# Performance work log

Hardware: AMD Instinct MI355X
Metric: run time of the kernel (lower is better)

Reference implementation:

```python
import jax, jax.numpy as jnp
import numpy as np

B, M, E, K = 8, 256, 128, 16
H, A, R, RMS = 1024, 256, 1024, 512
NEG = -1e25


def setup_inputs() -> dict:
    key = jax.random.key(0)
    ks = jax.random.split(key, 12)
    inp = {
        "mention_reprs": jax.random.normal(ks[0], (B, M, H), jnp.float32),
        "entities": jax.random.randint(ks[1], (B, E, K), 0, M),
        "entity_masks": jax.random.randint(ks[2], (B, E, K), 0, 2, dtype=jnp.int32),
        "relation_memory": jax.random.normal(ks[3], (R, RMS), jnp.float32),
        # GatedMILAttention params
        "Wv": jax.random.normal(ks[4], (A, H), jnp.float32) / np.sqrt(H),
        "bv": jnp.zeros((A,), jnp.float32),
        "Wu": jax.random.normal(ks[5], (A, H), jnp.float32) / np.sqrt(H),
        "bu": jnp.zeros((A,), jnp.float32),
        "Wa": jax.random.normal(ks[6], (1, A), jnp.float32) / np.sqrt(A),
        "ba": jnp.zeros((1,), jnp.float32),
        # relation memory read linear: Linear(RMS, H)
        "Wr": jax.random.normal(ks[7], (H, RMS), jnp.float32) / np.sqrt(RMS),
        "br": jnp.zeros((H,), jnp.float32),
        # output linear: Linear(H + RMS, H)
        "Wo": jax.random.normal(ks[8], (H, H + RMS), jnp.float32) / np.sqrt(H + RMS),
        "bo": jnp.zeros((H,), jnp.float32),
    }
    return inp


def reference(mention_reprs, entities, entity_masks, relation_memory,
              Wv, bv, Wu, bu, Wa, ba, Wr, br, Wo, bo):
    # gather mention clusters: [B, E, K, H]
    clusters = jax.vmap(lambda m, e: m[e])(mention_reprs, entities)
    # gated MIL attention
    aV = jnp.tanh(jnp.einsum('bekh,ah->beka', clusters, Wv) + bv)
    aU = jax.nn.sigmoid(jnp.einsum('bekh,ah->beka', clusters, Wu) + bu)
    logits = jnp.einsum('beka,oa->beko', aV * aU, Wa) + ba  # [B,E,K,1]
    mask = entity_masks[..., None].astype(bool)
    logits = jnp.where(mask, logits, NEG)
    a = jax.nn.softmax(logits, axis=2)
    # weighted pooling over mentions: [B, E, H]
    entity_reprs = jnp.sum(a * clusters, axis=2)
    # relation memory read (memory detached for the read projection)
    s_w = jax.lax.stop_gradient(relation_memory) @ Wr.T + br        # [R, H]
    s = jnp.einsum('beh,rh->ber', entity_reprs, s_w)                # [B, E, R]
    s = jnp.einsum('ber,rm->bem', s, relation_memory)               # [B, E, RMS]
    out = jnp.concatenate([entity_reprs, s], axis=-1) @ Wo.T + bo   # [B, E, H]
    return out  # dropout is identity at inference
```

## Files before the change

### kernel.cpp

```cpp
#include <hip/hip_runtime.h>
#include <cstdint>
#include <cstddef>

#define NEG_ (-1e25f)

typedef __bf16 bf16x8 __attribute__((ext_vector_type(8)));
typedef float  f32x4  __attribute__((ext_vector_type(4)));
typedef short  s16x8  __attribute__((ext_vector_type(8)));
typedef const __attribute__((address_space(1))) void* gas_t;
typedef __attribute__((address_space(3))) void* las_t;

#define MFMA16 __builtin_amdgcn_mfma_f32_16x16x32_bf16

__device__ __forceinline__ short f2bf(float f) {
  union { float f; unsigned u; } v; v.f = f;
  unsigned r = v.u + 0x7fffu + ((v.u >> 16) & 1u);
  return (short)(r >> 16);
}

__device__ __forceinline__ s16x8 cvt8(const float* s) {
  bf16x8 r;
  #pragma unroll
  for (int j = 0; j < 8; ++j) r[j] = (__bf16)s[j];
  union { bf16x8 b; s16x8 s; } u; u.b = r; return u.s;
}

struct Params {
  const float* ment; const int* ents; const int* msk;
  const float* rm; const float* Wv; const float* bv; const float* Wu;
  const float* bu; const float* Wa; const float* Wr; const float* br;
  const float* Wo; const float* bo; float* out;
  short *Xb, *Wvb, *Wub, *rmb, *Wrb, *Wo2b, *swTb, *Ub, *Weffb, *erb;
  float *wpart, *cf, *gw2;
};

__global__ __launch_bounds__(256) void k0(Params p) {
  const int g = blockIdx.x * 256 + threadIdx.x;
  #pragma unroll
  for (int it = 0; it < 4; ++it) {
    int u = g + it * 131072;
    long e = (long)u * 8;
    const float* src; short* dst;
    if (u < 262144)      { src = p.ment + e;                     dst = p.Xb + e; }
    else if (u < 294912) { long o = e - 2097152; src = p.Wv + o; dst = p.Wvb + o; }
    else if (u < 327680) { long o = e - 2359296; src = p.Wu + o; dst = p.Wub + o; }
    else if (u < 393216) { long o = e - 2621440; src = p.rm + o; dst = p.rmb + o; }
    else if (u < 458752) { long o = e - 3145728; src = p.Wr + o; dst = p.Wrb + o; }
    else                 { long o = e - 3670016;
                           src = p.Wo + (o >> 9) * 1536 + 1024 + (o & 511);
                           dst = p.Wo2b + o; }
    float t[8];
    *(float4*)t       = *(const float4*)src;
    *(float4*)(t + 4) = *(const float4*)(src + 4);
    *(s16x8*)dst = cvt8(t);
  }
}

__device__ void bgemm_dual(const short* __restrict__ A1, const short* __restrict__ A2,
                           long lda, const short* __restrict__ B, long ldb,
                           short* __restrict__ C1, short* __restrict__ C2, int ldc,
                           int NT, int m0, int n0, short* lds) {
  short* As1 = lds;
  short* As2 = lds + 4 * 2048;
  short* Bs  = lds + 8 * 2048;
  const int tid = threadIdx.x, wave = tid >> 6, lane = tid & 63;
  const int quad = lane >> 4, l16 = lane & 15;
  const int wm = (wave & 1) * 32, wn = (wave >> 1) * 32;
  const int srow = tid >> 2, scol = (tid & 3) * 8;
  const short* A1g = A1 + (long)(m0 + srow) * lda + scol;
  const short* A2g = A2 + (long)(m0 + srow) * lda + scol;
  const short* Bg  = B  + (long)(n0 + srow) * ldb + scol;
  const int ldsoff = wave * 512;
  auto issue = [&](int kt) {
    int buf = kt & 3; int ko = kt * 32;
    __builtin_amdgcn_global_load_lds((gas_t)(A1g + ko), (las_t)(As1 + buf * 2048 + ldsoff), 16, 0, 0);
    __builtin_amdgcn_global_load_lds((gas_t)(A2g + ko), (las_t)(As2 + buf * 2048 + ldsoff), 16, 0, 0);
    __builtin_amdgcn_global_load_lds((gas_t)(Bg  + ko), (las_t)(Bs  + buf * 2048 + ldsoff), 16, 0, 0);
  };
  f32x4 acc1[2][2] = {}, acc2[2][2] = {};
  issue(0); issue(1); issue(2);
  for (int kt = 0; kt < NT; ++kt) {
    int rem = NT - 1 - kt;
    if (rem >= 2)      asm volatile("s_waitcnt vmcnt(6)" ::: "memory");
    else if (rem == 1) asm volatile("s_waitcnt vmcnt(3)" ::: "memory");
    else               asm volatile("s_waitcnt vmcnt(0)" ::: "memory");
    asm volatile("s_barrier" ::: "memory");
    if (kt + 3 < NT) issue(kt + 3);
    const short* as1 = As1 + (kt & 3) * 2048;
    const short* as2 = As2 + (kt & 3) * 2048;
    const short* bs  = Bs  + (kt & 3) * 2048;
    bf16x8 a10 = *(const bf16x8*)&as1[(wm + l16) * 32 + quad * 8];
    bf16x8 a11 = *(const bf16x8*)&as1[(wm + 16 + l16) * 32 + quad * 8];
    bf16x8 a20 = *(const bf16x8*)&as2[(wm + l16) * 32 + quad * 8];
    bf16x8 a21 = *(const bf16x8*)&as2[(wm + 16 + l16) * 32 + quad * 8];
    bf16x8 b0  = *(const bf16x8*)&bs[(wn + l16) * 32 + quad * 8];
    bf16x8 b1  = *(const bf16x8*)&bs[(wn + 16 + l16) * 32 + quad * 8];
    acc1[0][0] = MFMA16(a10, b0, acc1[0][0], 0, 0, 0);
    acc1[0][1] = MFMA16(a10, b1, acc1[0][1], 0, 0, 0);
    acc1[1][0] = MFMA16(a11, b0, acc1[1][0], 0, 0, 0);
    acc1[1][1] = MFMA16(a11, b1, acc1[1][1], 0, 0, 0);
    acc2[0][0] = MFMA16(a20, b0, acc2[0][0], 0, 0, 0);
    acc2[0][1] = MFMA16(a20, b1, acc2[0][1], 0, 0, 0);
    acc2[1][0] = MFMA16(a21, b0, acc2[1][0], 0, 0, 0);
    acc2[1][1] = MFMA16(a21, b1, acc2[1][1], 0, 0, 0);
  }
  #pragma unroll
  for (int i = 0; i < 2; ++i)
    #pragma unroll
    for (int j = 0; j < 2; ++j) {
      int col = n0 + wn + j * 16 + l16;
      #pragma unroll
      for (int r = 0; r < 4; ++r) {
        int row = m0 + wm + i * 16 + quad * 4 + r;
        C1[(long)row * ldc + col] = f2bf(acc1[i][j][r]);
        C2[(long)row * ldc + col] = f2bf(acc2[i][j][r]);
      }
    }
}

template <int EPI>
__device__ void bgemm64(const short* __restrict__ A, int lda,
                        const short* __restrict__ B, int ldb,
                        void* __restrict__ C, int ldc, int NT, int m0, int n0,
                        const float* __restrict__ e0, const float* __restrict__ e1,
                        const float* __restrict__ e2, short* lds) {
  short* As = lds;
  short* Bs = lds + 4 * 2048;
  const int tid = threadIdx.x;
  const int wave = tid >> 6, lane = tid & 63;
  const int quad = lane >> 4, l16 = lane & 15;
  const int wm = (wave & 1) * 32, wn = (wave >> 1) * 32;
  const int srow = tid >> 2, scol = (tid & 3) * 8;
  const short* Ag = A + (long)(m0 + srow) * lda + scol;
  const short* Bg = B + (long)(n0 + srow) * ldb + scol;
  const int ldsoff = wave * 512;
  auto issue = [&](int kt) {
    int buf = kt & 3; int ko = kt * 32;
    __builtin_amdgcn_global_load_lds((gas_t)(Ag + ko), (las_t)(As + buf * 2048 + ldsoff), 16, 0, 0);
    __builtin_amdgcn_global_load_lds((gas_t)(Bg + ko), (las_t)(Bs + buf * 2048 + ldsoff), 16, 0, 0);
  };
  f32x4 acc[2][2] = {};
  issue(0); issue(1); issue(2);
  for (int kt = 0; kt < NT; ++kt) {
    int rem = NT - 1 - kt;
    if (rem >= 2)      asm volatile("s_waitcnt vmcnt(4)" ::: "memory");
    else if (rem == 1) asm volatile("s_waitcnt vmcnt(2)" ::: "memory");
    else               asm volatile("s_waitcnt vmcnt(0)" ::: "memory");
    asm volatile("s_barrier" ::: "memory");
    if (kt + 3 < NT) issue(kt + 3);
    const short* as = As + (kt & 3) * 2048;
    const short* bs = Bs + (kt & 3) * 2048;
    bf16x8 a0 = *(const bf16x8*)&as[(wm + l16) * 32 + quad * 8];
    bf16x8 a1 = *(const bf16x8*)&as[(wm + 16 + l16) * 32 + quad * 8];
    bf16x8 b0 = *(const bf16x8*)&bs[(wn + l16) * 32 + quad * 8];
    bf16x8 b1 = *(const bf16x8*)&bs[(wn + 16 + l16) * 32 + quad * 8];
    acc[0][0] = MFMA16(a0, b0, acc[0][0], 0, 0, 0);
    acc[0][1] = MFMA16(a0, b1, acc[0][1], 0, 0, 0);
    acc[1][0] = MFMA16(a1, b0, acc[1][0], 0, 0, 0);
    acc[1][1] = MFMA16(a1, b1, acc[1][1], 0, 0, 0);
  }
  #pragma unroll
  for (int i = 0; i < 2; ++i)
    #pragma unroll
    for (int j = 0; j < 2; ++j) {
      int col = n0 + wn + j * 16 + l16;
      #pragma unroll
      for (int r = 0; r < 4; ++r) {
        int row = m0 + wm + i * 16 + quad * 4 + r;
        float v = acc[i][j][r];
        if constexpr (EPI == 1) {
          v += e0[(long)row * 1536 + col];
          ((short*)C)[(long)row * ldc + col] = f2bf(v);
        } else {
          v += e0[col] + e1[row] * e2[col];
          ((float*)C)[(long)row * ldc + col] = v;
        }
      }
    }
}

__device__ void vu_ring(int mi, int ni, const Params& p, short* lds, float* red) {
  short* As  = lds;
  short* Bvs = lds + 4 * 1024;
  short* Bus = lds + 4 * 1024 + 4 * 2048;
  const int tid = threadIdx.x, wave = tid >> 6, lane = tid & 63;
  const int quad = lane >> 4, l16 = lane & 15;
  const int wm = (wave & 1) * 16, wn = (wave >> 1) * 32;
  const int m0 = mi * 32, n0 = ni * 64;
  const int srow = tid >> 2, scol = (tid & 3) * 8;
  const short* Ag  = p.Xb  + (long)(m0 + srow) * 1024 + scol;
  const short* Bvg = p.Wvb + (long)(n0 + srow) * 1024 + scol;
  const short* Bug = p.Wub + (long)(n0 + srow) * 1024 + scol;
  const int ldsoff = wave * 512;
  auto issue = [&](int kt) {
    int buf = kt & 3; int ko = kt * 32;
    if (wave < 2)
      __builtin_amdgcn_global_load_lds((gas_t)(Ag + ko), (las_t)(As + buf * 1024 + ldsoff), 16, 0, 0);
    __builtin_amdgcn_global_load_lds((gas_t)(Bvg + ko), (las_t)(Bvs + buf * 2048 + ldsoff), 16, 0, 0);
    __builtin_amdgcn_global_load_lds((gas_t)(Bug + ko), (las_t)(Bus + buf * 2048 + ldsoff), 16, 0, 0);
  };
  f32x4 accv[2] = {}, accu[2] = {};
  issue(0); issue(1); issue(2);
  for (int kt = 0; kt < 32; ++kt) {
    int rem = 31 - kt;
    if (wave < 2) {
      if (rem >= 2)      asm volatile("s_waitcnt vmcnt(6)" ::: "memory");
      else if (rem == 1) asm volatile("s_waitcnt vmcnt(3)" ::: "memory");
      else               asm volatile("s_waitcnt vmcnt(0)" ::: "memory");
    } else {
      if (rem >= 2)      asm volatile("s_waitcnt vmcnt(4)" ::: "memory");
      else if (rem == 1) asm volatile("s_waitcnt vmcnt(2)" ::: "memory");
      else               asm volatile("s_waitcnt vmcnt(0)" ::: "memory");
    }
    asm volatile("s_barrier" ::: "memory");
    if (kt + 3 < 32) issue(kt + 3);
    const short* as  = As  + (kt & 3) * 1024;
    const short* bvs = Bvs + (kt & 3) * 2048;
    const short* bus = Bus + (kt & 3) * 2048;
    bf16x8 af = *(const bf16x8*)&as[(wm + l16) * 32 + quad * 8];
    bf16x8 v0 = *(const bf16x8*)&bvs[(wn + l16) * 32 + quad * 8];
    bf16x8 v1 = *(const bf16x8*)&bvs[(wn + 16 + l16) * 32 + quad * 8];
    bf16x8 u0 = *(const bf16x8*)&bus[(wn + l16) * 32 + quad * 8];
    bf16x8 u1 = *(const bf16x8*)&bus[(wn + 16 + l16) * 32 + quad * 8];
    accv[0] = MFMA16(af, v0, accv[0], 0, 0, 0);
    accv[1] = MFMA16(af, v1, accv[1], 0, 0, 0);
    accu[0] = MFMA16(af, u0, accu[0], 0, 0, 0);
    accu[1] = MFMA16(af, u1, accu[1], 0, 0, 0);
  }
  float wsum[4] = {0.f, 0.f, 0.f, 0.f};
  #pragma unroll
  for (int j = 0; j < 2; ++j) {
    int col = n0 + wn + j * 16 + l16;
    float bvc = p.bv[col], buc = p.bu[col], wac = p.Wa[col];
    #pragma unroll
    for (int r = 0; r < 4; ++r) {
      float vv = tanhf(accv[j][r] + bvc);
      float uu = accu[j][r] + buc;
      wsum[r] += (vv / (1.0f + expf(-uu))) * wac;
    }
  }
  #pragma unroll
  for (int r = 0; r < 4; ++r) {
    float s = wsum[r];
    s += __shfl_down(s, 8, 16);
    s += __shfl_down(s, 4, 16);
    s += __shfl_down(s, 2, 16);
    s += __shfl_down(s, 1, 16);
    if (l16 == 0) red[(wave >> 1) * 32 + wm + quad * 4 + r] = s;
  }
  __syncthreads();
  if (tid < 32) p.wpart[ni * 2048 + m0 + tid] = red[tid] + red[32 + tid];
}

__device__ void gw2_wave(int row, const Params& p) {
  const int lane = threadIdx.x & 63;
  const short* u = p.Ub + (long)row * 1024 + lane * 16;
  union { s16x8 s; bf16x8 b; } w0, w1;
  w0.s = *(const s16x8*)u;
  w1.s = *(const s16x8*)(u + 8);
  float s = 0.f;
  #pragma unroll
  for (int j = 0; j < 8; ++j) s += (float)w0.b[j] + (float)w1.b[j];
  #pragma unroll
  for (int off = 32; off > 0; off >>= 1) s += __shfl_down(s, off);
  if (lane == 0) p.gw2[row] = s;
}

__device__ void entity_wave(int be, const Params& p) {
  const int lane = threadIdx.x & 63;
  const int b = be >> 7;
  float a = NEG_; int idx = 0;
  if (lane < 16) {
    idx = p.ents[be * 16 + lane];
    int j = (b << 8) + idx;
    float lw = p.wpart[j] + p.wpart[2048 + j] + p.wpart[4096 + j] + p.wpart[6144 + j];
    a = p.msk[be * 16 + lane] ? lw : NEG_;
  }
  float m = a;
  m = fmaxf(m, __shfl_xor(m, 1, 16));
  m = fmaxf(m, __shfl_xor(m, 2, 16));
  m = fmaxf(m, __shfl_xor(m, 4, 16));
  m = fmaxf(m, __shfl_xor(m, 8, 16));
  float e = expf(a - m);
  float s = e;
  s += __shfl_xor(s, 1, 16);
  s += __shfl_xor(s, 2, 16);
  s += __shfl_xor(s, 4, 16);
  s += __shfl_xor(s, 8, 16);
  float aw = e / s;
  const float* Xr = p.ment + ((long)b << 18);
  const int h0 = lane * 16;
  float acc[16];
  #pragma unroll
  for (int t = 0; t < 16; ++t) acc[t] = 0.f;
  #pragma unroll
  for (int k = 0; k < 16; ++k) {
    float ak = __shfl(aw, k);
    int   ik = __shfl(idx, k);
    const float* xr = Xr + (long)ik * 1024 + h0;
    f32x4 x0 = *(const f32x4*)(xr);
    f32x4 x1 = *(const f32x4*)(xr + 4);
    f32x4 x2 = *(const f32x4*)(xr + 8);
    f32x4 x3 = *(const f32x4*)(xr + 12);
    #pragma unroll
    for (int t = 0; t < 4; ++t) {
      acc[t]      += ak * x0[t];
      acc[4 + t]  += ak * x1[t];
      acc[8 + t]  += ak * x2[t];
      acc[12 + t] += ak * x3[t];
    }
  }
  short* er = p.erb + (long)be * 1024 + h0;
  *(s16x8*)er       = cvt8(acc);
  *(s16x8*)(er + 8) = cvt8(acc + 8);
  float c = 0.f;
  const float* brp = p.br + h0;
  #pragma unroll
  for (int t = 0; t < 16; ++t) c += acc[t] * brp[t];
  #pragma unroll
  for (int off = 32; off > 0; off >>= 1) c += __shfl_down(c, off);
  if (lane == 0) p.cf[be] = c;
}

__global__ __launch_bounds__(256) void k1(Params p) {
  __shared__ short lds[24576];
  __shared__ float red[64];
  const int blk = blockIdx.x;
  if (blk < 256) {
    bgemm_dual(p.Wrb, p.Wo2b, 512, p.rmb, 512, p.swTb, p.Ub, 1024, 16,
               (blk >> 4) * 64, (blk & 15) * 64, lds);
  } else {
    int q = blk - 256;
    vu_ring(q & 63, q >> 6, p, lds, red);
  }
}

__global__ __launch_bounds__(256) void k2(Params p) {
  __shared__ short lds[16384];
  const int blk = blockIdx.x;
  if (blk < 256) {
    bgemm64<1>(p.Ub, 1024, p.swTb, 1024, p.Weffb, 1024, 32,
               (blk >> 4) * 64, (blk & 15) * 64, p.Wo, nullptr, nullptr, lds);
  } else {
    int q = blk - 256;
    int wave = threadIdx.x >> 6;
    gw2_wave(q * 4 + wave, p);
    entity_wave(q * 4 + wave, p);
  }
}

__global__ __launch_bounds__(256) void k3(Params p) {
  __shared__ short lds[16384];
  const int blk = blockIdx.x;
  bgemm64<2>(p.erb, 1024, p.Weffb, 1024, p.out, 1024, 32,
             (blk >> 4) * 64, (blk & 15) * 64, p.bo, p.cf, p.gw2, lds);
}

extern "C" void kernel_launch(void* const* d_in, const int* in_sizes, int n_in,
                              void* d_out, int out_size, void* d_ws, size_t ws_size,
                              hipStream_t stream) {
  (void)in_sizes; (void)n_in; (void)out_size; (void)ws_size;
  Params p;
  p.ment = (const float*)d_in[0];
  p.ents = (const int*)d_in[1];
  p.msk  = (const int*)d_in[2];
  p.rm   = (const float*)d_in[3];
  p.Wv   = (const float*)d_in[4];
  p.bv   = (const float*)d_in[5];
  p.Wu   = (const float*)d_in[6];
  p.bu   = (const float*)d_in[7];
  p.Wa   = (const float*)d_in[8];
  p.Wr   = (const float*)d_in[10];
  p.br   = (const float*)d_in[11];
  p.Wo   = (const float*)d_in[12];
  p.bo   = (const float*)d_in[13];
  p.out  = (float*)d_out;

  char* w = (char*)d_ws;
  auto alloc = [&](size_t bytes) {
    void* q = (void*)w; w += (bytes + 255) & ~(size_t)255; return q;
  };
  p.Xb    = (short*)alloc((size_t)2048 * 1024 * 2);
  p.Wvb   = (short*)alloc((size_t)256 * 1024 * 2);
  p.Wub   = (short*)alloc((size_t)256 * 1024 * 2);
  p.rmb   = (short*)alloc((size_t)1024 * 512 * 2);
  p.Wrb   = (short*)alloc((size_t)1024 * 512 * 2);
  p.Wo2b  = (short*)alloc((size_t)1024 * 512 * 2);
  p.swTb  = (short*)alloc((size_t)1024 * 1024 * 2);
  p.Ub    = (short*)alloc((size_t)1024 * 1024 * 2);
  p.Weffb = (short*)alloc((size_t)1024 * 1024 * 2);
  p.erb   = (short*)alloc((size_t)1024 * 1024 * 2);
  p.wpart = (float*)alloc((size_t)4 * 2048 * 4);
  p.cf    = (float*)alloc((size_t)1024 * 4);
  p.gw2   = (float*)alloc((size_t)1024 * 4);

  k0<<<512, 256, 0, stream>>>(p);
  k1<<<512, 256, 0, stream>>>(p);
  k2<<<512, 256, 0, stream>>>(p);
  k3<<<256, 256, 0, stream>>>(p);
}
```

Before: 138.2 us.

## Fuse three dependent kernels into one persistent kernel with grid barriers

Merges k1, k2 and k3 into a single kernel, kF, that separates the stages with a software grid-wide barrier built from an atomic counter and a generation word. k0 resets the barrier state before kF runs. The aim is to remove two kernel launch gaps and the tail drain between stages. In exchange it needs all 512 blocks resident at once, which launch_bounds(256,2) and the larger LDS allocation must allow, otherwise it deadlocks. Half the blocks sit idle during the last GEMM stage.

```diff
diff --git a/kernel.cpp b/kernel.cpp
--- a/kernel.cpp
+++ b/kernel.cpp
@@ -32,9 +32,31 @@
   const float* Wo; const float* bo; float* out;
   short *Xb, *Wvb, *Wub, *rmb, *Wrb, *Wo2b, *swTb, *Ub, *Weffb, *erb;
   float *wpart, *cf, *gw2;
+  unsigned* bar;
 };
 
+__device__ __forceinline__ void gridbar(unsigned* bar, unsigned nb) {
+  __syncthreads();
+  if (threadIdx.x == 0) {
+    unsigned* cnt = bar;
+    unsigned* gen = bar + 16;
+    unsigned g = __hip_atomic_load(gen, __ATOMIC_RELAXED, __HIP_MEMORY_SCOPE_AGENT);
+    __threadfence();
+    unsigned v = __hip_atomic_fetch_add(cnt, 1u, __ATOMIC_ACQ_REL, __HIP_MEMORY_SCOPE_AGENT);
+    if (v == nb - 1u) {
+      __hip_atomic_store(cnt, 0u, __ATOMIC_RELAXED, __HIP_MEMORY_SCOPE_AGENT);
+      __hip_atomic_store(gen, g + 1u, __ATOMIC_RELEASE, __HIP_MEMORY_SCOPE_AGENT);
+    } else {
+      while (__hip_atomic_load(gen, __ATOMIC_ACQUIRE, __HIP_MEMORY_SCOPE_AGENT) == g)
+        __builtin_amdgcn_s_sleep(2);
+    }
+    __threadfence();
+  }
+  __syncthreads();
+}
+
 __global__ __launch_bounds__(256) void k0(Params p) {
+  if (blockIdx.x == 0 && threadIdx.x == 0) { p.bar[0] = 0u; p.bar[16] = 0u; }
   const int g = blockIdx.x * 256 + threadIdx.x;
   #pragma unroll
   for (int it = 0; it < 4; ++it) {
@@ -322,10 +344,11 @@
   if (lane == 0) p.cf[be] = c;
 }
 
-__global__ __launch_bounds__(256) void k1(Params p) {
+__global__ __launch_bounds__(256, 2) void kF(Params p) {
   __shared__ short lds[24576];
   __shared__ float red[64];
   const int blk = blockIdx.x;
+
   if (blk < 256) {
     bgemm_dual(p.Wrb, p.Wo2b, 512, p.rmb, 512, p.swTb, p.Ub, 1024, 16,
                (blk >> 4) * 64, (blk & 15) * 64, lds);
@@ -333,11 +356,8 @@
     int q = blk - 256;
     vu_ring(q & 63, q >> 6, p, lds, red);
   }
-}
-
-__global__ __launch_bounds__(256) void k2(Params p) {
-  __shared__ short lds[16384];
-  const int blk = blockIdx.x;
+  gridbar(p.bar, 512);
+
   if (blk < 256) {
     bgemm64<1>(p.Ub, 1024, p.swTb, 1024, p.Weffb, 1024, 32,
                (blk >> 4) * 64, (blk & 15) * 64, p.Wo, nullptr, nullptr, lds);
@@ -347,13 +367,12 @@
     gw2_wave(q * 4 + wave, p);
     entity_wave(q * 4 + wave, p);
   }
-}
-
-__global__ __launch_bounds__(256) void k3(Params p) {
-  __shared__ short lds[16384];
-  const int blk = blockIdx.x;
-  bgemm64<2>(p.erb, 1024, p.Weffb, 1024, p.out, 1024, 32,
-             (blk >> 4) * 64, (blk & 15) * 64, p.bo, p.cf, p.gw2, lds);
+  gridbar(p.bar, 512);
+
+  if (blk < 256) {
+    bgemm64<2>(p.erb, 1024, p.Weffb, 1024, p.out, 1024, 32,
+               (blk >> 4) * 64, (blk & 15) * 64, p.bo, p.cf, p.gw2, lds);
+  }
 }
 
 extern "C" void kernel_launch(void* const* d_in, const int* in_sizes, int n_in,
@@ -393,9 +412,8 @@
   p.wpart = (float*)alloc((size_t)4 * 2048 * 4);
   p.cf    = (float*)alloc((size_t)1024 * 4);
   p.gw2   = (float*)alloc((size_t)1024 * 4);
+  p.bar   = (unsigned*)alloc(256);
 
   k0<<<512, 256, 0, stream>>>(p);
-  k1<<<512, 256, 0, stream>>>(p);
-  k2<<<512, 256, 0, stream>>>(p);
-  k3<<<256, 256, 0, stream>>>(p);
-}
+  kF<<<512, 256, 0, stream>>>(p);
+}
```

New measurement: 366.4 us. 2.65x slower.

## Switch GEMMs to 128x128 tiles with 3-stage pipeline and enlarge VU tile

Applied to the files above, without the earlier changes.

Replaces the 64x64 GEMM tiles (and the dual-output GEMM) with a single 128x128 tile kernel where each wave computes a 64x64 sub-tile with a 3-buffer async LDS pipeline, and splits the dual GEMM into separate blocks. The gated attention GEMM tile grows from 32 rows to 128 rows. This raises MFMA work per LDS load and cuts global traffic, but reduces block counts (e.g. k3 to 64 blocks on a 256-CU GPU), risking underutilization and higher register pressure.

```diff
diff --git a/kernel.cpp b/kernel.cpp
--- a/kernel.cpp
+++ b/kernel.cpp
@@ -23,6 +23,10 @@
   #pragma unroll
   for (int j = 0; j < 8; ++j) r[j] = (__bf16)s[j];
   union { bf16x8 b; s16x8 s; } u; u.b = r; return u.s;
+}
+
+__device__ __forceinline__ void gload(const short* g, short* l) {
+  __builtin_amdgcn_global_load_lds((gas_t)g, (las_t)l, 16, 0, 0);
 }
 
 struct Params {
@@ -56,119 +60,63 @@
   }
 }
 
-__device__ void bgemm_dual(const short* __restrict__ A1, const short* __restrict__ A2,
-                           long lda, const short* __restrict__ B, long ldb,
-                           short* __restrict__ C1, short* __restrict__ C2, int ldc,
-                           int NT, int m0, int n0, short* lds) {
-  short* As1 = lds;
-  short* As2 = lds + 4 * 2048;
-  short* Bs  = lds + 8 * 2048;
+template <int NT, int EPI>
+__device__ void mm128(const short* __restrict__ A, int lda,
+                      const short* __restrict__ B, int ldb,
+                      void* __restrict__ C, int ldc, int m0, int n0,
+                      const float* __restrict__ e0, const float* __restrict__ e1,
+                      const float* __restrict__ e2, short* lds) {
+  short* As = lds;
+  short* Bs = lds + 12288;
   const int tid = threadIdx.x, wave = tid >> 6, lane = tid & 63;
   const int quad = lane >> 4, l16 = lane & 15;
-  const int wm = (wave & 1) * 32, wn = (wave >> 1) * 32;
-  const int srow = tid >> 2, scol = (tid & 3) * 8;
-  const short* A1g = A1 + (long)(m0 + srow) * lda + scol;
-  const short* A2g = A2 + (long)(m0 + srow) * lda + scol;
-  const short* Bg  = B  + (long)(n0 + srow) * ldb + scol;
-  const int ldsoff = wave * 512;
-  auto issue = [&](int kt) {
-    int buf = kt & 3; int ko = kt * 32;
-    __builtin_amdgcn_global_load_lds((gas_t)(A1g + ko), (las_t)(As1 + buf * 2048 + ldsoff), 16, 0, 0);
-    __builtin_amdgcn_global_load_lds((gas_t)(A2g + ko), (las_t)(As2 + buf * 2048 + ldsoff), 16, 0, 0);
-    __builtin_amdgcn_global_load_lds((gas_t)(Bg  + ko), (las_t)(Bs  + buf * 2048 + ldsoff), 16, 0, 0);
-  };
-  f32x4 acc1[2][2] = {}, acc2[2][2] = {};
-  issue(0); issue(1); issue(2);
-  for (int kt = 0; kt < NT; ++kt) {
-    int rem = NT - 1 - kt;
-    if (rem >= 2)      asm volatile("s_waitcnt vmcnt(6)" ::: "memory");
-    else if (rem == 1) asm volatile("s_waitcnt vmcnt(3)" ::: "memory");
-    else               asm volatile("s_waitcnt vmcnt(0)" ::: "memory");
-    asm volatile("s_barrier" ::: "memory");
-    if (kt + 3 < NT) issue(kt + 3);
-    const short* as1 = As1 + (kt & 3) * 2048;
-    const short* as2 = As2 + (kt & 3) * 2048;
-    const short* bs  = Bs  + (kt & 3) * 2048;
-    bf16x8 a10 = *(const bf16x8*)&as1[(wm + l16) * 32 + quad * 8];
-    bf16x8 a11 = *(const bf16x8*)&as1[(wm + 16 + l16) * 32 + quad * 8];
-    bf16x8 a20 = *(const bf16x8*)&as2[(wm + l16) * 32 + quad * 8];
-    bf16x8 a21 = *(const bf16x8*)&as2[(wm + 16 + l16) * 32 + quad * 8];
-    bf16x8 b0  = *(const bf16x8*)&bs[(wn + l16) * 32 + quad * 8];
-    bf16x8 b1  = *(const bf16x8*)&bs[(wn + 16 + l16) * 32 + quad * 8];
-    acc1[0][0] = MFMA16(a10, b0, acc1[0][0], 0, 0, 0);
-    acc1[0][1] = MFMA16(a10, b1, acc1[0][1], 0, 0, 0);
-    acc1[1][0] = MFMA16(a11, b0, acc1[1][0], 0, 0, 0);
-    acc1[1][1] = MFMA16(a11, b1, acc1[1][1], 0, 0, 0);
-    acc2[0][0] = MFMA16(a20, b0, acc2[0][0], 0, 0, 0);
-    acc2[0][1] = MFMA16(a20, b1, acc2[0][1], 0, 0, 0);
-    acc2[1][0] = MFMA16(a21, b0, acc2[1][0], 0, 0, 0);
-    acc2[1][1] = MFMA16(a21, b1, acc2[1][1], 0, 0, 0);
-  }
-  #pragma unroll
-  for (int i = 0; i < 2; ++i)
-    #pragma unroll
-    for (int j = 0; j < 2; ++j) {
-      int col = n0 + wn + j * 16 + l16;
-      #pragma unroll
-      for (int r = 0; r < 4; ++r) {
-        int row = m0 + wm + i * 16 + quad * 4 + r;
-        C1[(long)row * ldc + col] = f2bf(acc1[i][j][r]);
-        C2[(long)row * ldc + col] = f2bf(acc2[i][j][r]);
-      }
-    }
-}
-
-template <int EPI>
-__device__ void bgemm64(const short* __restrict__ A, int lda,
-                        const short* __restrict__ B, int ldb,
-                        void* __restrict__ C, int ldc, int NT, int m0, int n0,
-                        const float* __restrict__ e0, const float* __restrict__ e1,
-                        const float* __restrict__ e2, short* lds) {
-  short* As = lds;
-  short* Bs = lds + 4 * 2048;
-  const int tid = threadIdx.x;
-  const int wave = tid >> 6, lane = tid & 63;
-  const int quad = lane >> 4, l16 = lane & 15;
-  const int wm = (wave & 1) * 32, wn = (wave >> 1) * 32;
+  const int wm = (wave & 1) * 64, wn = (wave >> 1) * 64;
   const int srow = tid >> 2, scol = (tid & 3) * 8;
   const short* Ag = A + (long)(m0 + srow) * lda + scol;
   const short* Bg = B + (long)(n0 + srow) * ldb + scol;
-  const int ldsoff = wave * 512;
+  const int wb = wave * 512;
   auto issue = [&](int kt) {
-    int buf = kt & 3; int ko = kt * 32;
-    __builtin_amdgcn_global_load_lds((gas_t)(Ag + ko), (las_t)(As + buf * 2048 + ldsoff), 16, 0, 0);
-    __builtin_amdgcn_global_load_lds((gas_t)(Bg + ko), (las_t)(Bs + buf * 2048 + ldsoff), 16, 0, 0);
+    int buf = kt % 3; int ko = kt * 32;
+    gload(Ag + ko,            As + buf * 4096 + wb);
+    gload(Ag + 64 * lda + ko, As + buf * 4096 + 2048 + wb);
+    gload(Bg + ko,            Bs + buf * 4096 + wb);
+    gload(Bg + 64 * ldb + ko, Bs + buf * 4096 + 2048 + wb);
   };
-  f32x4 acc[2][2] = {};
-  issue(0); issue(1); issue(2);
+  f32x4 acc[4][4] = {};
+  issue(0); issue(1);
+  #pragma unroll
   for (int kt = 0; kt < NT; ++kt) {
-    int rem = NT - 1 - kt;
-    if (rem >= 2)      asm volatile("s_waitcnt vmcnt(4)" ::: "memory");
-    else if (rem == 1) asm volatile("s_waitcnt vmcnt(2)" ::: "memory");
-    else               asm volatile("s_waitcnt vmcnt(0)" ::: "memory");
+    if (kt < NT - 1) asm volatile("s_waitcnt vmcnt(4)" ::: "memory");
+    else             asm volatile("s_waitcnt vmcnt(0)" ::: "memory");
     asm volatile("s_barrier" ::: "memory");
-    if (kt + 3 < NT) issue(kt + 3);
-    const short* as = As + (kt & 3) * 2048;
-    const short* bs = Bs + (kt & 3) * 2048;
-    bf16x8 a0 = *(const bf16x8*)&as[(wm + l16) * 32 + quad * 8];
-    bf16x8 a1 = *(const bf16x8*)&as[(wm + 16 + l16) * 32 + quad * 8];
-    bf16x8 b0 = *(const bf16x8*)&bs[(wn + l16) * 32 + quad * 8];
-    bf16x8 b1 = *(const bf16x8*)&bs[(wn + 16 + l16) * 32 + quad * 8];
-    acc[0][0] = MFMA16(a0, b0, acc[0][0], 0, 0, 0);
-    acc[0][1] = MFMA16(a0, b1, acc[0][1], 0, 0, 0);
-    acc[1][0] = MFMA16(a1, b0, acc[1][0], 0, 0, 0);
-    acc[1][1] = MFMA16(a1, b1, acc[1][1], 0, 0, 0);
-  }
-  #pragma unroll
-  for (int i = 0; i < 2; ++i)
-    #pragma unroll
-    for (int j = 0; j < 2; ++j) {
+    if (kt + 2 < NT) issue(kt + 2);
+    const short* as = As + (kt % 3) * 4096;
+    const short* bs = Bs + (kt % 3) * 4096;
+    bf16x8 a[4], b[4];
+    #pragma unroll
+    for (int i = 0; i < 4; ++i)
+      a[i] = *(const bf16x8*)&as[(wm + i * 16 + l16) * 32 + quad * 8];
+    #pragma unroll
+    for (int j = 0; j < 4; ++j)
+      b[j] = *(const bf16x8*)&bs[(wn + j * 16 + l16) * 32 + quad * 8];
+    #pragma unroll
+    for (int i = 0; i < 4; ++i)
+      #pragma unroll
+      for (int j = 0; j < 4; ++j)
+        acc[i][j] = MFMA16(a[i], b[j], acc[i][j], 0, 0, 0);
+  }
+  #pragma unroll
+  for (int i = 0; i < 4; ++i)
+    #pragma unroll
+    for (int j = 0; j < 4; ++j) {
       int col = n0 + wn + j * 16 + l16;
       #pragma unroll
       for (int r = 0; r < 4; ++r) {
         int row = m0 + wm + i * 16 + quad * 4 + r;
         float v = acc[i][j][r];
-        if constexpr (EPI == 1) {
+        if constexpr (EPI == 0) {
+          ((short*)C)[(long)row * ldc + col] = f2bf(v);
+        } else if constexpr (EPI == 1) {
           v += e0[(long)row * 1536 + col];
           ((short*)C)[(long)row * ldc + col] = f2bf(v);
         } else {
@@ -179,77 +127,86 @@
     }
 }
 
-__device__ void vu_ring(int mi, int ni, const Params& p, short* lds, float* red) {
+__device__ void mmvu(int q, const Params& p, short* lds, float* red) {
   short* As  = lds;
-  short* Bvs = lds + 4 * 1024;
-  short* Bus = lds + 4 * 1024 + 4 * 2048;
+  short* Bvs = lds + 12288;
+  short* Bus = lds + 12288 + 6144;
+  const int mi = q >> 2, ni = q & 3;
+  const int m0 = mi * 128, n0 = ni * 64;
   const int tid = threadIdx.x, wave = tid >> 6, lane = tid & 63;
   const int quad = lane >> 4, l16 = lane & 15;
-  const int wm = (wave & 1) * 16, wn = (wave >> 1) * 32;
-  const int m0 = mi * 32, n0 = ni * 64;
+  const int wm = (wave & 1) * 64, wn = (wave >> 1) * 32;
   const int srow = tid >> 2, scol = (tid & 3) * 8;
   const short* Ag  = p.Xb  + (long)(m0 + srow) * 1024 + scol;
   const short* Bvg = p.Wvb + (long)(n0 + srow) * 1024 + scol;
   const short* Bug = p.Wub + (long)(n0 + srow) * 1024 + scol;
-  const int ldsoff = wave * 512;
+  const int wb = wave * 512;
   auto issue = [&](int kt) {
-    int buf = kt & 3; int ko = kt * 32;
-    if (wave < 2)
-      __builtin_amdgcn_global_load_lds((gas_t)(Ag + ko), (las_t)(As + buf * 1024 + ldsoff), 16, 0, 0);
-    __builtin_amdgcn_global_load_lds((gas_t)(Bvg + ko), (las_t)(Bvs + buf * 2048 + ldsoff), 16, 0, 0);
-    __builtin_amdgcn_global_load_lds((gas_t)(Bug + ko), (las_t)(Bus + buf * 2048 + ldsoff), 16, 0, 0);
+    int buf = kt % 3; int ko = kt * 32;
+    gload(Ag + ko,             As + buf * 4096 + wb);
+    gload(Ag + 64 * 1024 + ko, As + buf * 4096 + 2048 + wb);
+    gload(Bvg + ko,            Bvs + buf * 2048 + wb);
+    gload(Bug + ko,            Bus + buf * 2048 + wb);
   };
-  f32x4 accv[2] = {}, accu[2] = {};
-  issue(0); issue(1); issue(2);
+  f32x4 av[4][2] = {}, au[4][2] = {};
+  issue(0); issue(1);
+  #pragma unroll
   for (int kt = 0; kt < 32; ++kt) {
-    int rem = 31 - kt;
-    if (wave < 2) {
-      if (rem >= 2)      asm volatile("s_waitcnt vmcnt(6)" ::: "memory");
-      else if (rem == 1) asm volatile("s_waitcnt vmcnt(3)" ::: "memory");
-      else               asm volatile("s_waitcnt vmcnt(0)" ::: "memory");
-    } else {
-      if (rem >= 2)      asm volatile("s_waitcnt vmcnt(4)" ::: "memory");
-      else if (rem == 1) asm volatile("s_waitcnt vmcnt(2)" ::: "memory");
-      else               asm volatile("s_waitcnt vmcnt(0)" ::: "memory");
+    if (kt < 31) asm volatile("s_waitcnt vmcnt(4)" ::: "memory");
+    else         asm volatile("s_waitcnt vmcnt(0)" ::: "memory");
+    asm volatile("s_barrier" ::: "memory");
+    if (kt + 2 < 32) issue(kt + 2);
+    const short* as  = As  + (kt % 3) * 4096;
+    const short* bvs = Bvs + (kt % 3) * 2048;
+    const short* bus = Bus + (kt % 3) * 2048;
+    bf16x8 a[4], bv_[2], bu_[2];
+    #pragma unroll
+    for (int i = 0; i < 4; ++i)
+      a[i] = *(const bf16x8*)&as[(wm + i * 16 + l16) * 32 + quad * 8];
+    #pragma unroll
+    for (int j = 0; j < 2; ++j) {
+      bv_[j] = *(const bf16x8*)&bvs[(wn + j * 16 + l16) * 32 + quad * 8];
+      bu_[j] = *(const bf16x8*)&bus[(wn + j * 16 + l16) * 32 + quad * 8];
     }
-    asm volatile("s_barrier" ::: "memory");
-    if (kt + 3 < 32) issue(kt + 3);
-    const short* as  = As  + (kt & 3) * 1024;
-    const short* bvs = Bvs + (kt & 3) * 2048;
-    const short* bus = Bus + (kt & 3) * 2048;
-    bf16x8 af = *(const bf16x8*)&as[(wm + l16) * 32 + quad * 8];
-    bf16x8 v0 = *(const bf16x8*)&bvs[(wn + l16) * 32 + quad * 8];
-    bf16x8 v1 = *(const bf16x8*)&bvs[(wn + 16 + l16) * 32 + quad * 8];
-    bf16x8 u0 = *(const bf16x8*)&bus[(wn + l16) * 32 + quad * 8];
-    bf16x8 u1 = *(const bf16x8*)&bus[(wn + 16 + l16) * 32 + quad * 8];
-    accv[0] = MFMA16(af, v0, accv[0], 0, 0, 0);
-    accv[1] = MFMA16(af, v1, accv[1], 0, 0, 0);
-    accu[0] = MFMA16(af, u0, accu[0], 0, 0, 0);
-    accu[1] = MFMA16(af, u1, accu[1], 0, 0, 0);
-  }
-  float wsum[4] = {0.f, 0.f, 0.f, 0.f};
+    #pragma unroll
+    for (int i = 0; i < 4; ++i)
+      #pragma unroll
+      for (int j = 0; j < 2; ++j) {
+        av[i][j] = MFMA16(a[i], bv_[j], av[i][j], 0, 0, 0);
+        au[i][j] = MFMA16(a[i], bu_[j], au[i][j], 0, 0, 0);
+      }
+  }
+  float wsum[4][4];
+  #pragma unroll
+  for (int i = 0; i < 4; ++i)
+    #pragma unroll
+    for (int r = 0; r < 4; ++r) wsum[i][r] = 0.f;
   #pragma unroll
   for (int j = 0; j < 2; ++j) {
     int col = n0 + wn + j * 16 + l16;
     float bvc = p.bv[col], buc = p.bu[col], wac = p.Wa[col];
     #pragma unroll
+    for (int i = 0; i < 4; ++i)
+      #pragma unroll
+      for (int r = 0; r < 4; ++r) {
+        float vv = tanhf(av[i][j][r] + bvc);
+        float uu = au[i][j][r] + buc;
+        wsum[i][r] += (vv / (1.0f + expf(-uu))) * wac;
+      }
+  }
+  #pragma unroll
+  for (int i = 0; i < 4; ++i)
+    #pragma unroll
     for (int r = 0; r < 4; ++r) {
-      float vv = tanhf(accv[j][r] + bvc);
-      float uu = accu[j][r] + buc;
-      wsum[r] += (vv / (1.0f + expf(-uu))) * wac;
+      float s = wsum[i][r];
+      s += __shfl_down(s, 8, 16);
+      s += __shfl_down(s, 4, 16);
+      s += __shfl_down(s, 2, 16);
+      s += __shfl_down(s, 1, 16);
+      if (l16 == 0) red[(wave >> 1) * 128 + wm + i * 16 + quad * 4 + r] = s;
     }
-  }
-  #pragma unroll
-  for (int r = 0; r < 4; ++r) {
-    float s = wsum[r];
-    s += __shfl_down(s, 8, 16);
-    s += __shfl_down(s, 4, 16);
-    s += __shfl_down(s, 2, 16);
-    s += __shfl_down(s, 1, 16);
-    if (l16 == 0) red[(wave >> 1) * 32 + wm + quad * 4 + r] = s;
-  }
   __syncthreads();
-  if (tid < 32) p.wpart[ni * 2048 + m0 + tid] = red[tid] + red[32 + tid];
+  if (tid < 128) p.wpart[ni * 2048 + m0 + tid] = red[tid] + red[128 + tid];
 }
 
 __device__ void gw2_wave(int row, const Params& p) {
@@ -324,25 +281,29 @@
 
 __global__ __launch_bounds__(256) void k1(Params p) {
   __shared__ short lds[24576];
-  __shared__ float red[64];
+  __shared__ float red[256];
   const int blk = blockIdx.x;
-  if (blk < 256) {
-    bgemm_dual(p.Wrb, p.Wo2b, 512, p.rmb, 512, p.swTb, p.Ub, 1024, 16,
-               (blk >> 4) * 64, (blk & 15) * 64, lds);
+  if (blk < 64) {
+    mmvu(blk, p, lds, red);
+  } else if (blk < 128) {
+    int q = blk - 64;
+    mm128<16, 0>(p.Wrb, 512, p.rmb, 512, p.swTb, 1024,
+                 (q >> 3) * 128, (q & 7) * 128, nullptr, nullptr, nullptr, lds);
   } else {
-    int q = blk - 256;
-    vu_ring(q & 63, q >> 6, p, lds, red);
+    int q = blk - 128;
+    mm128<16, 0>(p.Wo2b, 512, p.rmb, 512, p.Ub, 1024,
+                 (q >> 3) * 128, (q & 7) * 128, nullptr, nullptr, nullptr, lds);
   }
 }
 
 __global__ __launch_bounds__(256) void k2(Params p) {
-  __shared__ short lds[16384];
+  __shared__ short lds[24576];
   const int blk = blockIdx.x;
-  if (blk < 256) {
-    bgemm64<1>(p.Ub, 1024, p.swTb, 1024, p.Weffb, 1024, 32,
-               (blk >> 4) * 64, (blk & 15) * 64, p.Wo, nullptr, nullptr, lds);
+  if (blk < 64) {
+    mm128<32, 1>(p.Ub, 1024, p.swTb, 1024, p.Weffb, 1024,
+                 (blk >> 3) * 128, (blk & 7) * 128, p.Wo, nullptr, nullptr, lds);
   } else {
-    int q = blk - 256;
+    int q = blk - 64;
     int wave = threadIdx.x >> 6;
     gw2_wave(q * 4 + wave, p);
     entity_wave(q * 4 + wave, p);
@@ -350,10 +311,10 @@
 }
 
 __global__ __launch_bounds__(256) void k3(Params p) {
-  __shared__ short lds[16384];
+  __shared__ short lds[24576];
   const int blk = blockIdx.x;
-  bgemm64<2>(p.erb, 1024, p.Weffb, 1024, p.out, 1024, 32,
-             (blk >> 4) * 64, (blk & 15) * 64, p.bo, p.cf, p.gw2, lds);
+  mm128<32, 2>(p.erb, 1024, p.Weffb, 1024, p.out, 1024,
+               (blk >> 3) * 128, (blk & 7) * 128, p.bo, p.cf, p.gw2, lds);
 }
 
 extern "C" void kernel_launch(void* const* d_in, const int* in_sizes, int n_in,
@@ -395,7 +356,7 @@
   p.gw2   = (float*)alloc((size_t)1024 * 4);
 
   k0<<<512, 256, 0, stream>>>(p);
-  k1<<<512, 256, 0, stream>>>(p);
-  k2<<<512, 256, 0, stream>>>(p);
-  k3<<<256, 256, 0, stream>>>(p);
-}
+  k1<<<192, 256, 0, stream>>>(p);
+  k2<<<320, 256, 0, stream>>>(p);
+  k3<<<64, 256, 0, stream>>>(p);
+}
```

Measured after the change: 156.7 us. 13.4% more time.

## Deepen GEMM prefetch pipelines, split dual GEMM into separate blocks, pre-convert Wo slice

Applied to the files above, without the earlier changes.

Replaces the dual-output GEMM in k1 with two independent 64x64 GEMM block sets, launching 768 blocks, and puts the vu_ring blocks first. The shared GEMM routine becomes a template with an 8-slot LDS ring and 6 tiles in flight, and vu_ring moves to a 6-slot ring with 4 tiles in flight. k0 also converts the first 1024 columns of Wo to bf16 so the k2 epilogue reads bf16 instead of strided fp32. The deeper pipelines are meant to hide global-load latency, at the cost of doubled LDS per block (64 KB), which may lower occupancy, and of reading the rm tile twice in k1.

```diff
diff --git a/kernel.cpp b/kernel.cpp
--- a/kernel.cpp
+++ b/kernel.cpp
@@ -18,11 +18,20 @@
   return (short)(r >> 16);
 }
 
+__device__ __forceinline__ float bf2f(short s) {
+  union { unsigned u; float f; } t; t.u = ((unsigned)(unsigned short)s) << 16;
+  return t.f;
+}
+
 __device__ __forceinline__ s16x8 cvt8(const float* s) {
   bf16x8 r;
   #pragma unroll
   for (int j = 0; j < 8; ++j) r[j] = (__bf16)s[j];
   union { bf16x8 b; s16x8 s; } u; u.b = r; return u.s;
+}
+
+__device__ __forceinline__ void gload(const short* g, short* l) {
+  __builtin_amdgcn_global_load_lds((gas_t)g, (las_t)l, 16, 0, 0);
 }
 
 struct Params {
@@ -30,14 +39,14 @@
   const float* rm; const float* Wv; const float* bv; const float* Wu;
   const float* bu; const float* Wa; const float* Wr; const float* br;
   const float* Wo; const float* bo; float* out;
-  short *Xb, *Wvb, *Wub, *rmb, *Wrb, *Wo2b, *swTb, *Ub, *Weffb, *erb;
+  short *Xb, *Wvb, *Wub, *rmb, *Wrb, *Wo2b, *Wo1b, *swTb, *Ub, *Weffb, *erb;
   float *wpart, *cf, *gw2;
 };
 
 __global__ __launch_bounds__(256) void k0(Params p) {
   const int g = blockIdx.x * 256 + threadIdx.x;
   #pragma unroll
-  for (int it = 0; it < 4; ++it) {
+  for (int it = 0; it < 5; ++it) {
     int u = g + it * 131072;
     long e = (long)u * 8;
     const float* src; short* dst;
@@ -46,9 +55,12 @@
     else if (u < 327680) { long o = e - 2359296; src = p.Wu + o; dst = p.Wub + o; }
     else if (u < 393216) { long o = e - 2621440; src = p.rm + o; dst = p.rmb + o; }
     else if (u < 458752) { long o = e - 3145728; src = p.Wr + o; dst = p.Wrb + o; }
-    else                 { long o = e - 3670016;
+    else if (u < 524288) { long o = e - 3670016;
                            src = p.Wo + (o >> 9) * 1536 + 1024 + (o & 511);
                            dst = p.Wo2b + o; }
+    else                 { long o = e - 4194304;
+                           src = p.Wo + (o >> 10) * 1536 + (o & 1023);
+                           dst = p.Wo1b + o; }
     float t[8];
     *(float4*)t       = *(const float4*)src;
     *(float4*)(t + 4) = *(const float4*)(src + 4);
@@ -56,100 +68,41 @@
   }
 }
 
-__device__ void bgemm_dual(const short* __restrict__ A1, const short* __restrict__ A2,
-                           long lda, const short* __restrict__ B, long ldb,
-                           short* __restrict__ C1, short* __restrict__ C2, int ldc,
-                           int NT, int m0, int n0, short* lds) {
-  short* As1 = lds;
-  short* As2 = lds + 4 * 2048;
-  short* Bs  = lds + 8 * 2048;
+template <int NT, int EPI>
+__device__ void g64(const short* __restrict__ A, int lda,
+                    const short* __restrict__ B, int ldb,
+                    void* __restrict__ C, int ldc, int m0, int n0,
+                    const short* __restrict__ w1, const float* __restrict__ e0,
+                    const float* __restrict__ e1, const float* __restrict__ e2,
+                    short* lds) {
+  short* As = lds;
+  short* Bs = lds + 16384;
   const int tid = threadIdx.x, wave = tid >> 6, lane = tid & 63;
-  const int quad = lane >> 4, l16 = lane & 15;
-  const int wm = (wave & 1) * 32, wn = (wave >> 1) * 32;
-  const int srow = tid >> 2, scol = (tid & 3) * 8;
-  const short* A1g = A1 + (long)(m0 + srow) * lda + scol;
-  const short* A2g = A2 + (long)(m0 + srow) * lda + scol;
-  const short* Bg  = B  + (long)(n0 + srow) * ldb + scol;
-  const int ldsoff = wave * 512;
-  auto issue = [&](int kt) {
-    int buf = kt & 3; int ko = kt * 32;
-    __builtin_amdgcn_global_load_lds((gas_t)(A1g + ko), (las_t)(As1 + buf * 2048 + ldsoff), 16, 0, 0);
-    __builtin_amdgcn_global_load_lds((gas_t)(A2g + ko), (las_t)(As2 + buf * 2048 + ldsoff), 16, 0, 0);
-    __builtin_amdgcn_global_load_lds((gas_t)(Bg  + ko), (las_t)(Bs  + buf * 2048 + ldsoff), 16, 0, 0);
-  };
-  f32x4 acc1[2][2] = {}, acc2[2][2] = {};
-  issue(0); issue(1); issue(2);
-  for (int kt = 0; kt < NT; ++kt) {
-    int rem = NT - 1 - kt;
-    if (rem >= 2)      asm volatile("s_waitcnt vmcnt(6)" ::: "memory");
-    else if (rem == 1) asm volatile("s_waitcnt vmcnt(3)" ::: "memory");
-    else               asm volatile("s_waitcnt vmcnt(0)" ::: "memory");
-    asm volatile("s_barrier" ::: "memory");
-    if (kt + 3 < NT) issue(kt + 3);
-    const short* as1 = As1 + (kt & 3) * 2048;
-    const short* as2 = As2 + (kt & 3) * 2048;
-    const short* bs  = Bs  + (kt & 3) * 2048;
-    bf16x8 a10 = *(const bf16x8*)&as1[(wm + l16) * 32 + quad * 8];
-    bf16x8 a11 = *(const bf16x8*)&as1[(wm + 16 + l16) * 32 + quad * 8];
-    bf16x8 a20 = *(const bf16x8*)&as2[(wm + l16) * 32 + quad * 8];
-    bf16x8 a21 = *(const bf16x8*)&as2[(wm + 16 + l16) * 32 + quad * 8];
-    bf16x8 b0  = *(const bf16x8*)&bs[(wn + l16) * 32 + quad * 8];
-    bf16x8 b1  = *(const bf16x8*)&bs[(wn + 16 + l16) * 32 + quad * 8];
-    acc1[0][0] = MFMA16(a10, b0, acc1[0][0], 0, 0, 0);
-    acc1[0][1] = MFMA16(a10, b1, acc1[0][1], 0, 0, 0);
-    acc1[1][0] = MFMA16(a11, b0, acc1[1][0], 0, 0, 0);
-    acc1[1][1] = MFMA16(a11, b1, acc1[1][1], 0, 0, 0);
-    acc2[0][0] = MFMA16(a20, b0, acc2[0][0], 0, 0, 0);
-    acc2[0][1] = MFMA16(a20, b1, acc2[0][1], 0, 0, 0);
-    acc2[1][0] = MFMA16(a21, b0, acc2[1][0], 0, 0, 0);
-    acc2[1][1] = MFMA16(a21, b1, acc2[1][1], 0, 0, 0);
-  }
-  #pragma unroll
-  for (int i = 0; i < 2; ++i)
-    #pragma unroll
-    for (int j = 0; j < 2; ++j) {
-      int col = n0 + wn + j * 16 + l16;
-      #pragma unroll
-      for (int r = 0; r < 4; ++r) {
-        int row = m0 + wm + i * 16 + quad * 4 + r;
-        C1[(long)row * ldc + col] = f2bf(acc1[i][j][r]);
-        C2[(long)row * ldc + col] = f2bf(acc2[i][j][r]);
-      }
-    }
-}
-
-template <int EPI>
-__device__ void bgemm64(const short* __restrict__ A, int lda,
-                        const short* __restrict__ B, int ldb,
-                        void* __restrict__ C, int ldc, int NT, int m0, int n0,
-                        const float* __restrict__ e0, const float* __restrict__ e1,
-                        const float* __restrict__ e2, short* lds) {
-  short* As = lds;
-  short* Bs = lds + 4 * 2048;
-  const int tid = threadIdx.x;
-  const int wave = tid >> 6, lane = tid & 63;
   const int quad = lane >> 4, l16 = lane & 15;
   const int wm = (wave & 1) * 32, wn = (wave >> 1) * 32;
   const int srow = tid >> 2, scol = (tid & 3) * 8;
   const short* Ag = A + (long)(m0 + srow) * lda + scol;
   const short* Bg = B + (long)(n0 + srow) * ldb + scol;
-  const int ldsoff = wave * 512;
+  const int wb = wave * 512;
   auto issue = [&](int kt) {
-    int buf = kt & 3; int ko = kt * 32;
-    __builtin_amdgcn_global_load_lds((gas_t)(Ag + ko), (las_t)(As + buf * 2048 + ldsoff), 16, 0, 0);
-    __builtin_amdgcn_global_load_lds((gas_t)(Bg + ko), (las_t)(Bs + buf * 2048 + ldsoff), 16, 0, 0);
+    int buf = kt & 7; int ko = kt * 32;
+    gload(Ag + ko, As + buf * 2048 + wb);
+    gload(Bg + ko, Bs + buf * 2048 + wb);
   };
   f32x4 acc[2][2] = {};
-  issue(0); issue(1); issue(2);
+  issue(0); issue(1); issue(2); issue(3); issue(4); issue(5);
   for (int kt = 0; kt < NT; ++kt) {
     int rem = NT - 1 - kt;
-    if (rem >= 2)      asm volatile("s_waitcnt vmcnt(4)" ::: "memory");
+    if (rem >= 5)      asm volatile("s_waitcnt vmcnt(10)" ::: "memory");
+    else if (rem == 4) asm volatile("s_waitcnt vmcnt(8)" ::: "memory");
+    else if (rem == 3) asm volatile("s_waitcnt vmcnt(6)" ::: "memory");
+    else if (rem == 2) asm volatile("s_waitcnt vmcnt(4)" ::: "memory");
     else if (rem == 1) asm volatile("s_waitcnt vmcnt(2)" ::: "memory");
     else               asm volatile("s_waitcnt vmcnt(0)" ::: "memory");
     asm volatile("s_barrier" ::: "memory");
-    if (kt + 3 < NT) issue(kt + 3);
-    const short* as = As + (kt & 3) * 2048;
-    const short* bs = Bs + (kt & 3) * 2048;
+    if (kt + 6 < NT) issue(kt + 6);
+    const short* as = As + (kt & 7) * 2048;
+    const short* bs = Bs + (kt & 7) * 2048;
     bf16x8 a0 = *(const bf16x8*)&as[(wm + l16) * 32 + quad * 8];
     bf16x8 a1 = *(const bf16x8*)&as[(wm + 16 + l16) * 32 + quad * 8];
     bf16x8 b0 = *(const bf16x8*)&bs[(wn + l16) * 32 + quad * 8];
@@ -168,8 +121,10 @@
       for (int r = 0; r < 4; ++r) {
         int row = m0 + wm + i * 16 + quad * 4 + r;
         float v = acc[i][j][r];
-        if constexpr (EPI == 1) {
-          v += e0[(long)row * 1536 + col];
+        if constexpr (EPI == 0) {
+          ((short*)C)[(long)row * ldc + col] = f2bf(v);
+        } else if constexpr (EPI == 1) {
+          v += bf2f(w1[(long)row * 1024 + col]);
           ((short*)C)[(long)row * ldc + col] = f2bf(v);
         } else {
           v += e0[col] + e1[row] * e2[col];
@@ -181,8 +136,8 @@
 
 __device__ void vu_ring(int mi, int ni, const Params& p, short* lds, float* red) {
   short* As  = lds;
-  short* Bvs = lds + 4 * 1024;
-  short* Bus = lds + 4 * 1024 + 4 * 2048;
+  short* Bvs = lds + 6 * 1024;
+  short* Bus = lds + 6 * 1024 + 6 * 2048;
   const int tid = threadIdx.x, wave = tid >> 6, lane = tid & 63;
   const int quad = lane >> 4, l16 = lane & 15;
   const int wm = (wave & 1) * 16, wn = (wave >> 1) * 32;
@@ -191,32 +146,34 @@
   const short* Ag  = p.Xb  + (long)(m0 + srow) * 1024 + scol;
   const short* Bvg = p.Wvb + (long)(n0 + srow) * 1024 + scol;
   const short* Bug = p.Wub + (long)(n0 + srow) * 1024 + scol;
-  const int ldsoff = wave * 512;
+  const int wb = wave * 512;
   auto issue = [&](int kt) {
-    int buf = kt & 3; int ko = kt * 32;
+    int buf = kt % 6; int ko = kt * 32;
     if (wave < 2)
-      __builtin_amdgcn_global_load_lds((gas_t)(Ag + ko), (las_t)(As + buf * 1024 + ldsoff), 16, 0, 0);
-    __builtin_amdgcn_global_load_lds((gas_t)(Bvg + ko), (las_t)(Bvs + buf * 2048 + ldsoff), 16, 0, 0);
-    __builtin_amdgcn_global_load_lds((gas_t)(Bug + ko), (las_t)(Bus + buf * 2048 + ldsoff), 16, 0, 0);
+      gload(Ag + ko, As + buf * 1024 + wb);
+    gload(Bvg + ko, Bvs + buf * 2048 + wb);
+    gload(Bug + ko, Bus + buf * 2048 + wb);
   };
   f32x4 accv[2] = {}, accu[2] = {};
-  issue(0); issue(1); issue(2);
+  issue(0); issue(1); issue(2); issue(3);
   for (int kt = 0; kt < 32; ++kt) {
     int rem = 31 - kt;
     if (wave < 2) {
-      if (rem >= 2)      asm volatile("s_waitcnt vmcnt(6)" ::: "memory");
+      if (rem >= 3)      asm volatile("s_waitcnt vmcnt(9)" ::: "memory");
+      else if (rem == 2) asm volatile("s_waitcnt vmcnt(6)" ::: "memory");
       else if (rem == 1) asm volatile("s_waitcnt vmcnt(3)" ::: "memory");
       else               asm volatile("s_waitcnt vmcnt(0)" ::: "memory");
     } else {
-      if (rem >= 2)      asm volatile("s_waitcnt vmcnt(4)" ::: "memory");
+      if (rem >= 3)      asm volatile("s_waitcnt vmcnt(6)" ::: "memory");
+      else if (rem == 2) asm volatile("s_waitcnt vmcnt(4)" ::: "memory");
       else if (rem == 1) asm volatile("s_waitcnt vmcnt(2)" ::: "memory");
       else               asm volatile("s_waitcnt vmcnt(0)" ::: "memory");
     }
     asm volatile("s_barrier" ::: "memory");
-    if (kt + 3 < 32) issue(kt + 3);
-    const short* as  = As  + (kt & 3) * 1024;
-    const short* bvs = Bvs + (kt & 3) * 2048;
-    const short* bus = Bus + (kt & 3) * 2048;
+    if (kt + 4 < 32) issue(kt + 4);
+    const short* as  = As  + (kt % 6) * 1024;
+    const short* bvs = Bvs + (kt % 6) * 2048;
+    const short* bus = Bus + (kt % 6) * 2048;
     bf16x8 af = *(const bf16x8*)&as[(wm + l16) * 32 + quad * 8];
     bf16x8 v0 = *(const bf16x8*)&bvs[(wn + l16) * 32 + quad * 8];
     bf16x8 v1 = *(const bf16x8*)&bvs[(wn + 16 + l16) * 32 + quad * 8];
@@ -323,24 +280,28 @@
 }
 
 __global__ __launch_bounds__(256) void k1(Params p) {
-  __shared__ short lds[24576];
+  __shared__ short lds[32768];
   __shared__ float red[64];
   const int blk = blockIdx.x;
   if (blk < 256) {
-    bgemm_dual(p.Wrb, p.Wo2b, 512, p.rmb, 512, p.swTb, p.Ub, 1024, 16,
-               (blk >> 4) * 64, (blk & 15) * 64, lds);
+    vu_ring(blk & 63, blk >> 6, p, lds, red);
+  } else if (blk < 512) {
+    int q = blk - 256;
+    g64<16, 0>(p.Wrb, 512, p.rmb, 512, p.swTb, 1024,
+               (q >> 4) * 64, (q & 15) * 64, nullptr, nullptr, nullptr, nullptr, lds);
   } else {
-    int q = blk - 256;
-    vu_ring(q & 63, q >> 6, p, lds, red);
+    int q = blk - 512;
+    g64<16, 0>(p.Wo2b, 512, p.rmb, 512, p.Ub, 1024,
+               (q >> 4) * 64, (q & 15) * 64, nullptr, nullptr, nullptr, nullptr, lds);
   }
 }
 
 __global__ __launch_bounds__(256) void k2(Params p) {
-  __shared__ short lds[16384];
+  __shared__ short lds[32768];
   const int blk = blockIdx.x;
   if (blk < 256) {
-    bgemm64<1>(p.Ub, 1024, p.swTb, 1024, p.Weffb, 1024, 32,
-               (blk >> 4) * 64, (blk & 15) * 64, p.Wo, nullptr, nullptr, lds);
+    g64<32, 1>(p.Ub, 1024, p.swTb, 1024, p.Weffb, 1024,
+               (blk >> 4) * 64, (blk & 15) * 64, p.Wo1b, nullptr, nullptr, nullptr, lds);
   } else {
     int q = blk - 256;
     int wave = threadIdx.x >> 6;
@@ -350,10 +311,10 @@
 }
 
 __global__ __launch_bounds__(256) void k3(Params p) {
-  __shared__ short lds[16384];
+  __shared__ short lds[32768];
   const int blk = blockIdx.x;
-  bgemm64<2>(p.erb, 1024, p.Weffb, 1024, p.out, 1024, 32,
-             (blk >> 4) * 64, (blk & 15) * 64, p.bo, p.cf, p.gw2, lds);
+  g64<32, 2>(p.erb, 1024, p.Weffb, 1024, p.out, 1024,
+             (blk >> 4) * 64, (blk & 15) * 64, nullptr, p.bo, p.cf, p.gw2, lds);
 }
 
 extern "C" void kernel_launch(void* const* d_in, const int* in_sizes, int n_in,
@@ -386,6 +347,7 @@
   p.rmb   = (short*)alloc((size_t)1024 * 512 * 2);
   p.Wrb   = (short*)alloc((size_t)1024 * 512 * 2);
   p.Wo2b  = (short*)alloc((size_t)1024 * 512 * 2);
+  p.Wo1b  = (short*)alloc((size_t)1024 * 1024 * 2);
   p.swTb  = (short*)alloc((size_t)1024 * 1024 * 2);
   p.Ub    = (short*)alloc((size_t)1024 * 1024 * 2);
   p.Weffb = (short*)alloc((size_t)1024 * 1024 * 2);
@@ -395,7 +357,7 @@
   p.gw2   = (float*)alloc((size_t)1024 * 4);
 
   k0<<<512, 256, 0, stream>>>(p);
-  k1<<<512, 256, 0, stream>>>(p);
+  k1<<<768, 256, 0, stream>>>(p);
   k2<<<512, 256, 0, stream>>>(p);
   k3<<<256, 256, 0, stream>>>(p);
 }
```

New measurement: 135.7 us. No clear change (-1.8%).
